# Kernel tuning notes

Hardware: AMD Instinct MI355X
Metric: run time of the kernel (lower is better)

Reference implementation:

```python
import jax, jax.numpy as jnp
import numpy as np

ALPHA = 0.5
SIGMA = 0.5
EPS = 1e-7

def setup_inputs() -> dict:
    key = jax.random.key(0)
    k1, k2, k3, k4 = jax.random.split(key, 4)
    n, T = 8192, 256
    return {
        "hazards": jax.random.normal(k1, (n, T), dtype=jnp.float32),
        "duration": jax.random.randint(k2, (n,), 0, T, dtype=jnp.int32),
        "event": jax.random.randint(k3, (n,), 0, 2, dtype=jnp.int32),
        "label": jax.random.randint(k4, (n,), 0, T, dtype=jnp.int32),
    }

def _deephit_loss(hazards, duration, event, label):
    dur = duration.reshape(-1)
    ev = event.reshape(-1)
    lab = label.reshape(-1)
    evf = ev.astype(hazards.dtype)

    # pair_rank_mat: R_ij = 1{D_i=1 and (T_i < T_j or (T_i == T_j and D_j = 0))}
    rank_mat = ((ev[:, None] != 0)
                & ((dur[:, None] < dur[None, :])
                   | ((dur[:, None] == dur[None, :]) & (ev[None, :] == 0)))
                ).astype(hazards.dtype)  # [n, n]

    # nll_pmf (pad_col adds a zero column -> T+1 bins)
    phi = jnp.pad(hazards, ((0, 0), (0, 1)))            # [n, T+1]
    gamma = jnp.max(phi, axis=1)                         # [n]
    cumsum = jnp.cumsum(jnp.exp(phi - gamma[:, None]), axis=1)  # [n, T+1]
    sum_ = cumsum[:, -1]
    phi_at = jnp.take_along_axis(phi, lab[:, None], axis=1)[:, 0]
    cum_at = jnp.take_along_axis(cumsum, lab[:, None], axis=1)[:, 0]
    part1 = (phi_at - gamma) * evf
    part2 = -jnp.log(jnp.maximum(sum_, 0.0) + EPS)
    part3 = jnp.log(jnp.maximum(sum_ - cum_at, 0.0) + EPS) * (1.0 - evf)
    nll = jnp.mean(-(part1 + part2 + part3))

    # rank_loss_deephit_single
    pmf = jax.nn.softmax(phi, axis=1)                    # [n, T+1]
    cdf = jnp.cumsum(pmf, axis=1)                        # [n, T+1]
    y = jax.nn.one_hot(lab, phi.shape[1], dtype=pmf.dtype)  # [n, T+1]
    r = cdf @ y.T                                        # r_ij = F_i(T_j), [n, n]
    diag_r = jnp.diagonal(r)                             # F_j(T_j)
    r = (diag_r[None, :] - r).T                          # r_ij = F_i(T_i) - F_j(T_i)
    rank_loss = jnp.mean(rank_mat * jnp.exp(-r / SIGMA))

    return ALPHA * nll + (1.0 - ALPHA) * rank_loss

def reference(hazards, duration, event, label):
    return _deephit_loss(hazards, duration, event, label)
```

## Files before the change

### kernel.cpp

```cpp
#include <hip/hip_runtime.h>
#include <hip/hip_fp16.h>

#define TBINS 256
#define RPB   32
#define NTHR  1024
#define EPS_F 1e-7f
#define INV_SIGMA 2.0f

__global__ __launch_bounds__(NTHR) void row_kernel(
    const float* __restrict__ hz, const int* __restrict__ ev,
    const int* __restrict__ lab,
    __half* __restrict__ WT, float* __restrict__ rowA,
    float* __restrict__ nllpart, float* __restrict__ accR, int* __restrict__ done,
    int n)
{
    __shared__ float trs[RPB][261];
    __shared__ float nllred[RPB];

    const int tid  = threadIdx.x;
    const int wid  = tid >> 6;
    const int lane = tid & 63;

    if (blockIdx.x == 0 && tid == 0) { *accR = 0.f; *done = 0; }

    #pragma unroll
    for (int r = 0; r < 2; ++r) {
        const int lrow = wid * 2 + r;
        const int row  = blockIdx.x * RPB + lrow;
        const bool act = row < n;
        const int rrow = act ? row : 0;

        const float4 v = ((const float4*)(hz + (size_t)rrow * TBINS))[lane];

        float m = fmaxf(fmaxf(v.x, v.y), fmaxf(v.z, v.w));
        #pragma unroll
        for (int off = 32; off; off >>= 1) m = fmaxf(m, __shfl_xor(m, off));
        const float gamma = fmaxf(m, 0.0f);

        const float e0 = expf(v.x - gamma), e1 = expf(v.y - gamma);
        const float e2 = expf(v.z - gamma), e3 = expf(v.w - gamma);
        const float local = e0 + e1 + e2 + e3;

        float pre = local;
        #pragma unroll
        for (int off = 1; off < 64; off <<= 1) {
            float tv = __shfl_up(pre, off);
            if (lane >= off) pre += tv;
        }
        const float excl  = pre - local;
        const float total = __shfl(pre, 63);
        const float sum_  = total + expf(-gamma);
        const float c0 = excl + e0, c1 = c0 + e1, c2 = c1 + e2, c3 = c2 + e3;

        const int L = lab[rrow];
        const int e = ev[rrow];
        const int sel = L & 3;
        float csel = (sel == 0) ? c0 : (sel == 1) ? c1 : (sel == 2) ? c2 : c3;
        const float cum_at = __shfl(csel, L >> 2);
        const float inv = 1.0f / sum_;

        float4 w;
        w.x = expf(c0 * inv * INV_SIGMA);
        w.y = expf(c1 * inv * INV_SIGMA);
        w.z = expf(c2 * inv * INV_SIGMA);
        w.w = expf(c3 * inv * INV_SIGMA);
        *(float4*)&trs[lrow][4 * lane] = w;

        if (lane == 0) {
            float nll_i = 0.f, a_i = 0.f;
            if (act) {
                const float phi_at = hz[(size_t)row * TBINS + L];
                const float evf = (float)e;
                const float p1 = (phi_at - gamma) * evf;
                const float p2 = -logf(fmaxf(sum_, 0.f) + EPS_F);
                const float p3 = logf(fmaxf(sum_ - cum_at, 0.f) + EPS_F) * (1.f - evf);
                nll_i = -(p1 + p2 + p3);
                a_i = e ? expf(-(cum_at * inv) * INV_SIGMA) : 0.f;
                rowA[row] = a_i;
            }
            nllred[lrow] = nll_i;
        }
    }
    __syncthreads();

    if (tid == 0) {
        float s = 0.f;
        #pragma unroll
        for (int k = 0; k < RPB; ++k) s += nllred[k];
        nllpart[blockIdx.x] = s;
    }

    #pragma unroll
    for (int k = 0; k < 2; ++k) {
        const int t = (tid >> 3) + 128 * k;
        const int j = tid & 7;
        const int i0 = blockIdx.x * RPB + 4 * j;
        if (i0 + 3 < n) {
            ushort4 p;
            p.x = __half_as_ushort(__float2half(trs[4 * j + 0][t]));
            p.y = __half_as_ushort(__float2half(trs[4 * j + 1][t]));
            p.z = __half_as_ushort(__float2half(trs[4 * j + 2][t]));
            p.w = __half_as_ushort(__float2half(trs[4 * j + 3][t]));
            *(ushort4*)&WT[(size_t)t * n + i0] = p;
        }
    }
}

__global__ __launch_bounds__(NTHR) void agg_rank_kernel(
    const __half* __restrict__ WT, const int* __restrict__ dur,
    const int* __restrict__ ev, const int* __restrict__ lab,
    const float* __restrict__ rowA, const float* __restrict__ nllpart,
    float* __restrict__ accR, int* __restrict__ done,
    float* __restrict__ out, int n, int nblk1)
{
    __shared__ float hist[16][512];
    __shared__ float comb[512];
    __shared__ float Brow[TBINS];
    __shared__ float red[16];
    __shared__ int lastflag;

    const int t    = blockIdx.x;
    const int tid  = threadIdx.x;
    const int wid  = tid >> 6;
    const int lane = tid & 63;

    for (int i = tid; i < 16 * 512; i += NTHR) ((float*)hist)[i] = 0.f;
    __syncthreads();

    {
        const __half* w = WT + (size_t)t * n;
        const int i0 = tid * 8;
        if (i0 + 7 < n) {
            const ushort4 ha = *(const ushort4*)&w[i0];
            const ushort4 hb = *(const ushort4*)&w[i0 + 4];
            const int4 da = *(const int4*)&dur[i0];
            const int4 db = *(const int4*)&dur[i0 + 4];
            const int4 ea = *(const int4*)&ev[i0];
            const int4 eb = *(const int4*)&ev[i0 + 4];
            float* hb_ = hist[wid];
            atomicAdd(&hb_[da.x + (ea.x << 8)], __half2float(__ushort_as_half(ha.x)));
            atomicAdd(&hb_[da.y + (ea.y << 8)], __half2float(__ushort_as_half(ha.y)));
            atomicAdd(&hb_[da.z + (ea.z << 8)], __half2float(__ushort_as_half(ha.z)));
            atomicAdd(&hb_[da.w + (ea.w << 8)], __half2float(__ushort_as_half(ha.w)));
            atomicAdd(&hb_[db.x + (eb.x << 8)], __half2float(__ushort_as_half(hb.x)));
            atomicAdd(&hb_[db.y + (eb.y << 8)], __half2float(__ushort_as_half(hb.y)));
            atomicAdd(&hb_[db.z + (eb.z << 8)], __half2float(__ushort_as_half(hb.z)));
            atomicAdd(&hb_[db.w + (eb.w << 8)], __half2float(__ushort_as_half(hb.w)));
        }
    }
    __syncthreads();

    if (tid < 512) {
        float s = 0.f;
        #pragma unroll
        for (int k = 0; k < 16; ++k) s += hist[k][tid];
        comb[tid] = s;
    }
    __syncthreads();

    if (tid < 64) {
        const int d0 = tid * 4;
        const float g0 = comb[d0 + 0] + comb[d0 + 256];
        const float g1 = comb[d0 + 1] + comb[d0 + 257];
        const float g2 = comb[d0 + 2] + comb[d0 + 258];
        const float g3 = comb[d0 + 3] + comb[d0 + 259];
        const float c0 = g0, c1 = c0 + g1, c2 = c1 + g2, c3 = c2 + g3;
        float pre = c3;
        #pragma unroll
        for (int off = 1; off < 64; off <<= 1) {
            float tv = __shfl_up(pre, off);
            if (tid >= off) pre += tv;
        }
        const float excl = pre - c3;
        const float tot  = __shfl(pre, 63);
        Brow[d0 + 0] = (tot - (excl + c0)) + comb[d0 + 0];
        Brow[d0 + 1] = (tot - (excl + c1)) + comb[d0 + 1];
        Brow[d0 + 2] = (tot - (excl + c2)) + comb[d0 + 2];
        Brow[d0 + 3] = (tot - (excl + c3)) + comb[d0 + 3];
    }
    __syncthreads();

    float val = 0.f;
    {
        const int i0 = tid * 8;
        if (i0 + 7 < n) {
            const int4 la = *(const int4*)&lab[i0];
            const int4 lb = *(const int4*)&lab[i0 + 4];
            const int ls[8] = { la.x, la.y, la.z, la.w, lb.x, lb.y, lb.z, lb.w };
            #pragma unroll
            for (int k = 0; k < 8; ++k) {
                if (ls[k] == t) {
                    const float a = rowA[i0 + k];
                    if (a != 0.f) val += a * Brow[dur[i0 + k]];
                }
            }
        }
    }
    #pragma unroll
    for (int off = 32; off; off >>= 1) val += __shfl_xor(val, off);
    if (lane == 0) red[wid] = val;
    __syncthreads();

    if (tid == 0) {
        float s = 0.f;
        #pragma unroll
        for (int k = 0; k < 16; ++k) s += red[k];
        atomicAdd(accR, s);
        __threadfence();
        const int old = atomicAdd(done, 1);
        lastflag = (old == (int)gridDim.x - 1) ? 1 : 0;
    }
    __syncthreads();

    if (lastflag) {
        float s = (tid < nblk1) ? nllpart[tid] : 0.f;
        #pragma unroll
        for (int off = 32; off; off >>= 1) s += __shfl_xor(s, off);
        if (lane == 0) red[wid] = s;
        __syncthreads();
        if (tid == 0) {
            float S = 0.f;
            #pragma unroll
            for (int k = 0; k < 16; ++k) S += red[k];
            __threadfence();
            const float R = atomicAdd(accR, 0.0f);
            const double nll = (double)S / (double)n;
            const double rl  = (double)R / ((double)n * (double)n);
            out[0] = (float)(0.5 * nll + 0.5 * rl);
        }
    }
}

extern "C" void kernel_launch(void* const* d_in, const int* in_sizes, int n_in,
                              void* d_out, int out_size, void* d_ws, size_t ws_size,
                              hipStream_t stream) {
    const float* hz  = (const float*)d_in[0];
    const int*   dur = (const int*)d_in[1];
    const int*   ev  = (const int*)d_in[2];
    const int*   lab = (const int*)d_in[3];
    float* out = (float*)d_out;

    const int n = in_sizes[1];
    const int nblk1 = (n + RPB - 1) / RPB;

    __half* WT      = (__half*)d_ws;
    float*  rowA    = (float*)(WT + (size_t)TBINS * n);
    float*  nllpart = rowA + n;
    float*  accR    = nllpart + nblk1;
    int*    done    = (int*)(accR + 1);

    row_kernel<<<nblk1, NTHR, 0, stream>>>(hz, ev, lab, WT, rowA, nllpart, accR, done, n);
    agg_rank_kernel<<<TBINS, NTHR, 0, stream>>>(WT, dur, ev, lab, rowA, nllpart,
                                                accR, done, out, n, nblk1);
}
```

Before: 88.33 us.

## Pack per-row dur/label/event into one aux word and halve histogram copies

The row kernel now writes a packed 32-bit aux word (duration, label, event) plus a half-precision rowA. The aggregation kernel reads one uint4 pair instead of separate dur/ev/lab int4 loads, and reuses those values for the label-match pass. phi_at now comes from a warp shuffle instead of a global reload. Shared histogram copies drop from 16 to 8, so two waves share each copy, which lowers zeroing and reduction work but adds atomic contention. Storing rowA as fp16 costs a little precision, and a scalar tail path is added for n not divisible by 8.

```diff
diff --git a/kernel.cpp b/kernel.cpp
--- a/kernel.cpp
+++ b/kernel.cpp
@@ -4,15 +4,16 @@
 #define TBINS 256
 #define RPB   32
 #define NTHR  1024
+#define NHIST 8
 #define EPS_F 1e-7f
 #define INV_SIGMA 2.0f
 
 __global__ __launch_bounds__(NTHR) void row_kernel(
-    const float* __restrict__ hz, const int* __restrict__ ev,
-    const int* __restrict__ lab,
-    __half* __restrict__ WT, float* __restrict__ rowA,
-    float* __restrict__ nllpart, float* __restrict__ accR, int* __restrict__ done,
-    int n)
+    const float* __restrict__ hz, const int* __restrict__ dur,
+    const int* __restrict__ ev,  const int* __restrict__ lab,
+    __half* __restrict__ WT, __half* __restrict__ rowAh,
+    unsigned* __restrict__ aux, float* __restrict__ nllpart,
+    float* __restrict__ accR, int* __restrict__ done, int n)
 {
     __shared__ float trs[RPB][261];
     __shared__ float nllred[RPB];
@@ -54,9 +55,12 @@
 
         const int L = lab[rrow];
         const int e = ev[rrow];
+        const int d = dur[rrow];
         const int sel = L & 3;
-        float csel = (sel == 0) ? c0 : (sel == 1) ? c1 : (sel == 2) ? c2 : c3;
+        const float csel  = (sel == 0) ? c0  : (sel == 1) ? c1  : (sel == 2) ? c2  : c3;
+        const float phsel = (sel == 0) ? v.x : (sel == 1) ? v.y : (sel == 2) ? v.z : v.w;
         const float cum_at = __shfl(csel, L >> 2);
+        const float phi_at = __shfl(phsel, L >> 2);
         const float inv = 1.0f / sum_;
 
         float4 w;
@@ -67,16 +71,16 @@
         *(float4*)&trs[lrow][4 * lane] = w;
 
         if (lane == 0) {
-            float nll_i = 0.f, a_i = 0.f;
+            float nll_i = 0.f;
             if (act) {
-                const float phi_at = hz[(size_t)row * TBINS + L];
                 const float evf = (float)e;
                 const float p1 = (phi_at - gamma) * evf;
                 const float p2 = -logf(fmaxf(sum_, 0.f) + EPS_F);
                 const float p3 = logf(fmaxf(sum_ - cum_at, 0.f) + EPS_F) * (1.f - evf);
                 nll_i = -(p1 + p2 + p3);
-                a_i = e ? expf(-(cum_at * inv) * INV_SIGMA) : 0.f;
-                rowA[row] = a_i;
+                const float a_i = e ? expf(-(cum_at * inv) * INV_SIGMA) : 0.f;
+                rowAh[row] = __float2half(a_i);
+                aux[row] = (unsigned)d | ((unsigned)L << 8) | ((unsigned)(e != 0) << 16);
             }
             nllred[lrow] = nll_i;
         }
@@ -107,13 +111,12 @@
 }
 
 __global__ __launch_bounds__(NTHR) void agg_rank_kernel(
-    const __half* __restrict__ WT, const int* __restrict__ dur,
-    const int* __restrict__ ev, const int* __restrict__ lab,
-    const float* __restrict__ rowA, const float* __restrict__ nllpart,
+    const __half* __restrict__ WT, const unsigned* __restrict__ aux,
+    const __half* __restrict__ rowAh, const float* __restrict__ nllpart,
     float* __restrict__ accR, int* __restrict__ done,
     float* __restrict__ out, int n, int nblk1)
 {
-    __shared__ float hist[16][512];
+    __shared__ float hist[NHIST][512];
     __shared__ float comb[512];
     __shared__ float Brow[TBINS];
     __shared__ float red[16];
@@ -124,28 +127,32 @@
     const int wid  = tid >> 6;
     const int lane = tid & 63;
 
-    for (int i = tid; i < 16 * 512; i += NTHR) ((float*)hist)[i] = 0.f;
-    __syncthreads();
-
-    {
-        const __half* w = WT + (size_t)t * n;
-        const int i0 = tid * 8;
-        if (i0 + 7 < n) {
-            const ushort4 ha = *(const ushort4*)&w[i0];
-            const ushort4 hb = *(const ushort4*)&w[i0 + 4];
-            const int4 da = *(const int4*)&dur[i0];
-            const int4 db = *(const int4*)&dur[i0 + 4];
-            const int4 ea = *(const int4*)&ev[i0];
-            const int4 eb = *(const int4*)&ev[i0 + 4];
-            float* hb_ = hist[wid];
-            atomicAdd(&hb_[da.x + (ea.x << 8)], __half2float(__ushort_as_half(ha.x)));
-            atomicAdd(&hb_[da.y + (ea.y << 8)], __half2float(__ushort_as_half(ha.y)));
-            atomicAdd(&hb_[da.z + (ea.z << 8)], __half2float(__ushort_as_half(ha.z)));
-            atomicAdd(&hb_[da.w + (ea.w << 8)], __half2float(__ushort_as_half(ha.w)));
-            atomicAdd(&hb_[db.x + (eb.x << 8)], __half2float(__ushort_as_half(hb.x)));
-            atomicAdd(&hb_[db.y + (eb.y << 8)], __half2float(__ushort_as_half(hb.y)));
-            atomicAdd(&hb_[db.z + (eb.z << 8)], __half2float(__ushort_as_half(hb.z)));
-            atomicAdd(&hb_[db.w + (eb.w << 8)], __half2float(__ushort_as_half(hb.w)));
+    for (int i = tid; i < NHIST * 512; i += NTHR) ((float*)hist)[i] = 0.f;
+    __syncthreads();
+
+    const __half* w = WT + (size_t)t * n;
+    const int i0 = tid * 8;
+    const bool full = (i0 + 7 < n);
+    unsigned ax[8];
+    if (full) {
+        const ushort4 ha = *(const ushort4*)&w[i0];
+        const ushort4 hb = *(const ushort4*)&w[i0 + 4];
+        const uint4 xa = *(const uint4*)&aux[i0];
+        const uint4 xb = *(const uint4*)&aux[i0 + 4];
+        ax[0] = xa.x; ax[1] = xa.y; ax[2] = xa.z; ax[3] = xa.w;
+        ax[4] = xb.x; ax[5] = xb.y; ax[6] = xb.z; ax[7] = xb.w;
+        const unsigned short hs[8] = { ha.x, ha.y, ha.z, ha.w, hb.x, hb.y, hb.z, hb.w };
+        float* hp = hist[wid >> 1];
+        #pragma unroll
+        for (int k = 0; k < 8; ++k) {
+            const int bin = (int)(ax[k] & 255u) | ((int)((ax[k] >> 16) & 1u) << 8);
+            atomicAdd(&hp[bin], __half2float(__ushort_as_half(hs[k])));
+        }
+    } else {
+        for (int i = i0; i < n; ++i) {
+            const unsigned x = aux[i];
+            const int bin = (int)(x & 255u) | ((int)((x >> 16) & 1u) << 8);
+            atomicAdd(&hist[wid >> 1][bin], __half2float(w[i]));
         }
     }
     __syncthreads();
@@ -153,7 +160,7 @@
     if (tid < 512) {
         float s = 0.f;
         #pragma unroll
-        for (int k = 0; k < 16; ++k) s += hist[k][tid];
+        for (int k = 0; k < NHIST; ++k) s += hist[k][tid];
         comb[tid] = s;
     }
     __syncthreads();
@@ -181,18 +188,20 @@
     __syncthreads();
 
     float val = 0.f;
-    {
-        const int i0 = tid * 8;
-        if (i0 + 7 < n) {
-            const int4 la = *(const int4*)&lab[i0];
-            const int4 lb = *(const int4*)&lab[i0 + 4];
-            const int ls[8] = { la.x, la.y, la.z, la.w, lb.x, lb.y, lb.z, lb.w };
-            #pragma unroll
-            for (int k = 0; k < 8; ++k) {
-                if (ls[k] == t) {
-                    const float a = rowA[i0 + k];
-                    if (a != 0.f) val += a * Brow[dur[i0 + k]];
-                }
+    if (full) {
+        #pragma unroll
+        for (int k = 0; k < 8; ++k) {
+            if ((int)((ax[k] >> 8) & 255u) == t) {
+                const float a = __half2float(rowAh[i0 + k]);
+                if (a != 0.f) val += a * Brow[ax[k] & 255u];
+            }
+        }
+    } else {
+        for (int i = i0; i < n; ++i) {
+            const unsigned x = aux[i];
+            if ((int)((x >> 8) & 255u) == t) {
+                const float a = __half2float(rowAh[i]);
+                if (a != 0.f) val += a * Brow[x & 255u];
             }
         }
     }
@@ -243,13 +252,15 @@
     const int n = in_sizes[1];
     const int nblk1 = (n + RPB - 1) / RPB;
 
-    __half* WT      = (__half*)d_ws;
-    float*  rowA    = (float*)(WT + (size_t)TBINS * n);
-    float*  nllpart = rowA + n;
-    float*  accR    = nllpart + nblk1;
-    int*    done    = (int*)(accR + 1);
-
-    row_kernel<<<nblk1, NTHR, 0, stream>>>(hz, ev, lab, WT, rowA, nllpart, accR, done, n);
-    agg_rank_kernel<<<TBINS, NTHR, 0, stream>>>(WT, dur, ev, lab, rowA, nllpart,
+    __half*   WT      = (__half*)d_ws;
+    __half*   rowAh   = WT + (size_t)TBINS * n;
+    unsigned* aux     = (unsigned*)(rowAh + n);
+    float*    nllpart = (float*)(aux + n);
+    float*    accR    = nllpart + nblk1;
+    int*      done    = (int*)(accR + 1);
+
+    row_kernel<<<nblk1, NTHR, 0, stream>>>(hz, dur, ev, lab, WT, rowAh, aux,
+                                           nllpart, accR, done, n);
+    agg_rank_kernel<<<TBINS, NTHR, 0, stream>>>(WT, aux, rowAh, nllpart,
                                                 accR, done, out, n, nblk1);
 }
```

Result: no change. 88.34 us (+0.0%).
